# Kernel optimization log

Measured on AMD Instinct MI355X. Metric: run time of the kernel, lower is better.

## Reference

```python
import jax, jax.numpy as jnp
import numpy as np

D = 128        # feature_dims
ITERS = 2      # update_iters
B, R = 8, 256  # n segments (proteins), residues per segment
NEG_SLOPE = 0.1

def leaky(x):
    return jax.nn.leaky_relu(x, NEG_SLOPE)

def setup_inputs() -> dict:
    key = jax.random.key(0)
    ks = jax.random.split(key, 13)
    def w(k, shape):
        fan_in = shape[0]
        return jax.random.normal(k, shape, jnp.float32) / np.sqrt(fan_in)
    return {
        "fresidues": jax.random.normal(ks[0], (B, R, 20), jnp.float32),
        "coordinates": jax.random.normal(ks[1], (B, R, 3), jnp.float32) * 10.0,
        "W_emb": w(ks[2], (20, D)),                    # res_embedding (no bias)
        "W_e1": w(ks[3], (2 * D + 1, D)),              # linear_e layer 1
        "b_e1": jnp.zeros((D,), jnp.float32),
        "W_e2": w(ks[4], (D, D)),                      # linear_e layer 2
        "b_e2": jnp.zeros((D,), jnp.float32),
        "W_inf": w(ks[5], (D, 1)),                     # linear_inf gate
        "b_inf": jnp.zeros((1,), jnp.float32),
        "W_h1": w(ks[6], (2 * D, D)),                  # linear_h layer 1
        "b_h1": jnp.zeros((D,), jnp.float32),
        "W_h2": w(ks[7], (D, D)),                      # linear_h layer 2
        "b_h2": jnp.zeros((D,), jnp.float32),
    }

def reference(fresidues, coordinates, W_emb, W_e1, b_e1, W_e2, b_e2,
              W_inf, b_inf, W_h1, b_h1, W_h2, b_h2):
    # h: [B,R,D]
    h = leaky(fresidues @ W_emb)
    # pairwise squared distances: [B,R,R,1], constant across iterations
    d2 = jnp.sum(jnp.square(coordinates[:, :, None, :] - coordinates[:, None, :, :]),
                 axis=-1, keepdims=True)
    # mask out self-edges (1 - eye): [1,R,R,1]
    mask = (1.0 - jnp.eye(R, dtype=h.dtype))[None, :, :, None]
    # split edge-MLP first-layer weights to avoid materializing the [B,R,R,2D+1] concat:
    # m_input = cat([h_i, h_j, d2]) @ W_e1  ==  h_i@W_i + h_j@W_j + d2*w_d
    W_i, W_j, w_d = W_e1[:D], W_e1[D:2 * D], W_e1[2 * D]
    for _ in range(ITERS):
        ti = h @ W_i                                   # [B,R,D] receiver part
        tj = h @ W_j                                   # [B,R,D] sender part
        pre = ti[:, :, None, :] + tj[:, None, :, :] + d2 * w_d + b_e1  # [B,R,R,D]
        m = leaky(leaky(pre) @ W_e2 + b_e2)            # [B,R,R,D]
        e = jax.nn.sigmoid(m @ W_inf + b_inf) * mask   # [B,R,R,1]
        m_pre = jnp.sum(m * e, axis=2)                 # sum over senders j -> [B,R,D]
        hm = jnp.concatenate([h, m_pre], axis=-1)      # [B,R,2D]
        h = (leaky(hm @ W_h1 + b_h1) @ W_h2 + b_h2) + h
    return h

if __name__ == "__main__":
    out = reference(**setup_inputs())
    print(out.shape, out.dtype)
```

## Files before the change

kernel.cpp:

```cpp
#include <hip/hip_runtime.h>

typedef unsigned short ushort_t;
typedef __attribute__((ext_vector_type(8))) short shortx8;
typedef __attribute__((ext_vector_type(4))) float floatx4;
typedef __attribute__((ext_vector_type(2))) float floatx2;

#define NS 0.1f

__device__ __forceinline__ ushort_t f2bf_rne(float f) {
  union { float f; unsigned int u; } v; v.f = f;
  unsigned int r = v.u + 0x7FFFu + ((v.u >> 16) & 1u);
  return (ushort_t)(r >> 16);
}
__device__ __forceinline__ unsigned int pk2bf(float a, float b) {
  union { float f; unsigned int u; } x, y; x.f = a; y.f = b;
  return __builtin_amdgcn_perm(y.u + 0x8000u, x.u + 0x8000u, 0x07060302u);
}
__device__ __forceinline__ unsigned int cvtpk_bf16(float a, float b) {
  unsigned int r;
  asm("v_cvt_pk_bf16_f32 %0, %1, %2" : "=v"(r) : "v"(a), "v"(b));
  return r;
}
__device__ __forceinline__ ushort_t f2bf_rhu(float f) {
  union { float f; unsigned int u; } v; v.f = f;
  return (ushort_t)((v.u + 0x8000u) >> 16);
}
__device__ __forceinline__ float lk(float x) { return fmaxf(x, NS * x); }
__device__ __forceinline__ floatx2 lk2(floatx2 v) {
  return __builtin_elementwise_max(v, v * (floatx2){NS, NS});
}

__global__ __launch_bounds__(256) void prep_w(
    const float* __restrict__ W_e1, const float* __restrict__ W_e2,
    const float* __restrict__ W_h1, const float* __restrict__ W_h2,
    ushort_t* __restrict__ wijf, ushort_t* __restrict__ we2f,
    ushort_t* __restrict__ wh1f, ushort_t* __restrict__ wh2f) {
  int e = blockIdx.x * 256 + threadIdx.x;
  int which, le;
  if (e < 32768) { which = 0; le = e; }
  else if (e < 49152) { which = 1; le = e - 32768; }
  else if (e < 81920) { which = 2; le = e - 49152; }
  else { which = 3; le = e - 81920; }
  const int NT = (which == 0) ? 16 : 8;
  int f = le >> 3, j = le & 7;
  int lane = f & 63, ft = f >> 6;
  int t = ft % NT, s = ft / NT;
  int n = t * 16 + (lane & 15), k = s * 32 + (lane >> 4) * 8 + j;
  float v; ushort_t* d;
  if (which == 0) { v = (n < 128) ? W_e1[k * 128 + n] : W_e1[(128 + k) * 128 + (n - 128)]; d = wijf; }
  else if (which == 1) { v = W_e2[k * 128 + n]; d = we2f; }
  else if (which == 2) { v = W_h1[k * 128 + n]; d = wh1f; }
  else { v = W_h2[k * 128 + n]; d = wh2f; }
  d[le] = f2bf_rne(v);
}

__device__ __forceinline__ void proj_store(float v, int m, int n,
                                           float* __restrict__ ti, float* __restrict__ tjf) {
  if (n < 128) {
    ti[(size_t)m * 128 + n] = v;
  } else {
    int k = n - 128, b = m >> 8, j = m & 255;
    int s = k >> 5, lg2 = (k >> 3) & 3, j8 = k & 7;
    tjf[((((size_t)(b * 4 + s)) * 256 + j) * 4 + lg2) * 8 + j8] = v;
  }
}

__global__ __launch_bounds__(256) void h0_proj(
    const float* __restrict__ fres, const float* __restrict__ Wemb,
    const ushort_t* __restrict__ wijf, float* __restrict__ h_out,
    float* __restrict__ ti, float* __restrict__ tjf) {
  const int m0 = blockIdx.x * 16;
  const int tid = threadIdx.x;
  const int w = tid >> 6, lane = tid & 63, l16 = lane & 15, lg = lane >> 4;
  __shared__ __align__(16) ushort_t sH[16][136];
  {
    const int row = tid >> 4, c0 = (tid & 15) * 8;
    const float* fr = fres + (size_t)(m0 + row) * 20;
    float a[8] = {0, 0, 0, 0, 0, 0, 0, 0};
    for (int k = 0; k < 20; ++k) {
      float fv = fr[k];
      float4 w0 = *(const float4*)(Wemb + k * 128 + c0);
      float4 w1 = *(const float4*)(Wemb + k * 128 + c0 + 4);
      a[0] += fv * w0.x; a[1] += fv * w0.y; a[2] += fv * w0.z; a[3] += fv * w0.w;
      a[4] += fv * w1.x; a[5] += fv * w1.y; a[6] += fv * w1.z; a[7] += fv * w1.w;
    }
#pragma unroll
    for (int x = 0; x < 8; ++x) a[x] = lk(a[x]);
    float* ho = h_out + (size_t)(m0 + row) * 128 + c0;
    *(float4*)ho = (float4){a[0], a[1], a[2], a[3]};
    *(float4*)(ho + 4) = (float4){a[4], a[5], a[6], a[7]};
    unsigned int* sh = (unsigned int*)&sH[row][c0];
    sh[0] = pk2bf(a[0], a[1]); sh[1] = pk2bf(a[2], a[3]);
    sh[2] = pk2bf(a[4], a[5]); sh[3] = pk2bf(a[6], a[7]);
  }
  __syncthreads();
  floatx4 ap[4];
#pragma unroll
  for (int q = 0; q < 4; ++q) ap[q] = (floatx4){0.f, 0.f, 0.f, 0.f};
  const shortx8* Wp = (const shortx8*)wijf;
#pragma unroll
  for (int s = 0; s < 4; ++s) {
    shortx8 af = *(const shortx8*)&sH[l16][s * 32 + lg * 8];
#pragma unroll
    for (int q = 0; q < 4; ++q)
      ap[q] = __builtin_amdgcn_mfma_f32_16x16x32_bf16(af, Wp[(s * 16 + 4 * w + q) * 64 + lane], ap[q], 0, 0, 0);
  }
#pragma unroll
  for (int q = 0; q < 4; ++q) {
    const int n = (4 * w + q) * 16 + l16;
#pragma unroll
    for (int r = 0; r < 4; ++r) proj_store(ap[q][r], m0 + lg * 4 + r, n, ti, tjf);
  }
}

__global__ __launch_bounds__(512, 4) void edge_kernel(
    const float* __restrict__ ti, const float* __restrict__ tjf,
    const float* __restrict__ coords, const ushort_t* __restrict__ we2f,
    const float* __restrict__ W_e1, const float* __restrict__ b_e1,
    const float* __restrict__ b_e2, const float* __restrict__ W_inf,
    const float* __restrict__ b_inf, float* __restrict__ mp) {
  const int blk = blockIdx.x;
  const int b = blk >> 8, i = blk & 255;
  const int tid = threadIdx.x;
  const int w = tid >> 6, lane = tid & 63, l16 = lane & 15, lg = lane >> 4;

  __shared__ __align__(16) ushort_t sW[16384];
  __shared__ __align__(16) float sTiP[128];
  __shared__ __align__(16) float sWd[128];
  __shared__ __align__(16) float sD2[256];
  __shared__ __align__(16) float sMp[8][128];

  {
    shortx8* dst = (shortx8*)sW;
    const shortx8* src = (const shortx8*)we2f;
#pragma unroll
    for (int r = 0; r < 4; ++r) dst[r * 512 + tid] = src[r * 512 + tid];
  }
  if (tid < 128) {
    sTiP[tid] = ti[(size_t)(b * 256 + i) * 128 + tid] + b_e1[tid];
    sWd[tid] = W_e1[256 * 128 + tid];
  } else if (tid >= 256) {
    const int j = tid - 256;
    float dx = coords[(size_t)(b * 256 + i) * 3 + 0] - coords[(size_t)(b * 256 + j) * 3 + 0];
    float dy = coords[(size_t)(b * 256 + i) * 3 + 1] - coords[(size_t)(b * 256 + j) * 3 + 1];
    float dz = coords[(size_t)(b * 256 + i) * 3 + 2] - coords[(size_t)(b * 256 + j) * 3 + 2];
    sD2[j] = dx * dx + dy * dy + dz * dz;
  }
  floatx4 acc[2][8];
#pragma unroll
  for (int t = 0; t < 8; ++t) {
    float bv = b_e2[t * 16 + l16];
    acc[0][t] = (floatx4){bv, bv, bv, bv};
    acc[1][t] = acc[0][t];
  }
  __syncthreads();

  float d2a[2];
  d2a[0] = sD2[w * 16 + l16];
  d2a[1] = sD2[128 + w * 16 + l16];
  const shortx8* sWf = (const shortx8*)sW;

#pragma unroll
  for (int s = 0; s < 4; ++s) {
    const int k0 = s * 32 + lg * 8;
    floatx2 p2[4], w2[4];
#pragma unroll
    for (int x = 0; x < 4; ++x) {
      p2[x] = *(const floatx2*)&sTiP[k0 + 2 * x];
      w2[x] = *(const floatx2*)&sWd[k0 + 2 * x];
    }
    shortx8 af[2];
#pragma unroll
    for (int c = 0; c < 2; ++c) {
      const int jr = c * 128 + w * 16 + l16;
      const float* tb = tjf + (((size_t)(b * 4 + s) * 256 + jr) * 4 + lg) * 8;
      float4 t0 = *(const float4*)tb;
      float4 t1 = *(const float4*)(tb + 4);
      const floatx2 d2v = (floatx2){d2a[c], d2a[c]};
      floatx2 l0 = lk2((floatx2){t0.x, t0.y} + (p2[0] + d2v * w2[0]));
      floatx2 l1 = lk2((floatx2){t0.z, t0.w} + (p2[1] + d2v * w2[1]));
      floatx2 l2 = lk2((floatx2){t1.x, t1.y} + (p2[2] + d2v * w2[2]));
      floatx2 l3 = lk2((floatx2){t1.z, t1.w} + (p2[3] + d2v * w2[3]));
      union { shortx8 s8; unsigned int u[4]; } A;
      A.u[0] = cvtpk_bf16(l0.x, l0.y); A.u[1] = cvtpk_bf16(l1.x, l1.y);
      A.u[2] = cvtpk_bf16(l2.x, l2.y); A.u[3] = cvtpk_bf16(l3.x, l3.y);
      af[c] = A.s8;
    }
#pragma unroll
    for (int tg = 0; tg < 2; ++tg) {
      shortx8 b0 = sWf[(s * 8 + tg * 4 + 0) * 64 + lane];
      shortx8 b1 = sWf[(s * 8 + tg * 4 + 1) * 64 + lane];
      shortx8 b2 = sWf[(s * 8 + tg * 4 + 2) * 64 + lane];
      shortx8 b3 = sWf[(s * 8 + tg * 4 + 3) * 64 + lane];
      __builtin_amdgcn_s_setprio(1);
#pragma unroll
      for (int c = 0; c < 2; ++c) {
        acc[c][tg * 4 + 0] = __builtin_amdgcn_mfma_f32_16x16x32_bf16(af[c], b0, acc[c][tg * 4 + 0], 0, 0, 0);
        acc[c][tg * 4 + 1] = __builtin_amdgcn_mfma_f32_16x16x32_bf16(af[c], b1, acc[c][tg * 4 + 1], 0, 0, 0);
        acc[c][tg * 4 + 2] = __builtin_amdgcn_mfma_f32_16x16x32_bf16(af[c], b2, acc[c][tg * 4 + 2], 0, 0, 0);
        acc[c][tg * 4 + 3] = __builtin_amdgcn_mfma_f32_16x16x32_bf16(af[c], b3, acc[c][tg * 4 + 3], 0, 0, 0);
      }
      __builtin_amdgcn_s_setprio(0);
    }
  }

  float winfv[8], mpacc[8];
#pragma unroll
  for (int t = 0; t < 8; ++t) { winfv[t] = W_inf[t * 16 + l16]; mpacc[t] = 0.f; }
  const float binf = b_inf[0];
#pragma unroll
  for (int c = 0; c < 2; ++c) {
#pragma unroll
    for (int t = 0; t < 8; ++t) {
      floatx2 v0 = lk2((floatx2){acc[c][t][0], acc[c][t][1]});
      floatx2 v1 = lk2((floatx2){acc[c][t][2], acc[c][t][3]});
      acc[c][t][0] = v0.x; acc[c][t][1] = v0.y; acc[c][t][2] = v1.x; acc[c][t][3] = v1.y;
    }
    float p[4];
#pragma unroll
    for (int r = 0; r < 4; ++r) {
      float sum = 0.f;
#pragma unroll
      for (int t = 0; t < 8; ++t) sum += acc[c][t][r] * winfv[t];
      p[r] = sum;
    }
#pragma unroll
    for (int off = 1; off <= 8; off <<= 1)
#pragma unroll
      for (int r = 0; r < 4; ++r) p[r] += __shfl_xor(p[r], off);
#pragma unroll
    for (int r = 0; r < 4; ++r) {
      const int jg = c * 128 + w * 16 + lg * 4 + r;
      float x = p[r] + binf;
      float e = __builtin_amdgcn_rcpf(1.f + __expf(-x));
      if (jg == i) e = 0.f;
#pragma unroll
      for (int t = 0; t < 8; ++t) mpacc[t] += acc[c][t][r] * e;
    }
  }
#pragma unroll
  for (int t = 0; t < 8; ++t) {
    mpacc[t] += __shfl_xor(mpacc[t], 16);
    mpacc[t] += __shfl_xor(mpacc[t], 32);
  }
  if (lg == 0) {
#pragma unroll
    for (int t = 0; t < 8; ++t) sMp[w][t * 16 + l16] = mpacc[t];
  }
  __syncthreads();
  if (tid < 128) {
    float v = sMp[0][tid] + sMp[1][tid] + sMp[2][tid] + sMp[3][tid]
            + sMp[4][tid] + sMp[5][tid] + sMp[6][tid] + sMp[7][tid];
    mp[(size_t)(b * 256 + i) * 128 + tid] = v;
  }
}

__global__ __launch_bounds__(256) void node_kernel(
    const float* __restrict__ h_in, const float* __restrict__ mp,
    const ushort_t* __restrict__ wh1f, const float* __restrict__ b_h1,
    const ushort_t* __restrict__ wh2f, const float* __restrict__ b_h2,
    const ushort_t* __restrict__ wijf, float* __restrict__ h_out,
    float* __restrict__ ti, float* __restrict__ tjf, const int do_proj) {
  const int m0 = blockIdx.x * 16;
  const int tid = threadIdx.x;
  const int w = tid >> 6, lane = tid & 63, l16 = lane & 15, lg = lane >> 4;
  __shared__ __align__(16) ushort_t sA[16][264];
  __shared__ __align__(16) ushort_t sU[16][136];
  __shared__ __align__(16) ushort_t sHp[16][136];

  {
    const int row = tid >> 4, c0 = (tid & 15) * 16;
    unsigned int* dst = (unsigned int*)&sA[row][c0];
    if (c0 < 128) {
      const float* src = h_in + (size_t)(m0 + row) * 128 + c0;
#pragma unroll
      for (int x = 0; x < 8; ++x) dst[x] = pk2bf(src[2 * x], src[2 * x + 1]);
    } else {
      const float* s0 = mp + (size_t)(m0 + row) * 128 + (c0 - 128);
#pragma unroll
      for (int x = 0; x < 8; ++x) dst[x] = pk2bf(s0[2 * x], s0[2 * x + 1]);
    }
  }
  __syncthreads();
  floatx4 au[2];
#pragma unroll
  for (int q = 0; q < 2; ++q) { float bv = b_h1[(2 * w + q) * 16 + l16]; au[q] = (floatx4){bv, bv, bv, bv}; }
  const shortx8* W1 = (const shortx8*)wh1f;
#pragma unroll
  for (int s = 0; s < 8; ++s) {
    shortx8 af = *(const shortx8*)&sA[l16][s * 32 + lg * 8];
#pragma unroll
    for (int q = 0; q < 2; ++q)
      au[q] = __builtin_amdgcn_mfma_f32_16x16x32_bf16(af, W1[(s * 8 + 2 * w + q) * 64 + lane], au[q], 0, 0, 0);
  }
#pragma unroll
  for (int q = 0; q < 2; ++q)
#pragma unroll
    for (int r = 0; r < 4; ++r)
      sU[lg * 4 + r][(2 * w + q) * 16 + l16] = f2bf_rhu(lk(au[q][r]));
  __syncthreads();
  floatx4 ah[2];
#pragma unroll
  for (int q = 0; q < 2; ++q) { float bv = b_h2[(2 * w + q) * 16 + l16]; ah[q] = (floatx4){bv, bv, bv, bv}; }
  const shortx8* W2 = (const shortx8*)wh2f;
#pragma unroll
  for (int s = 0; s < 4; ++s) {
    shortx8 af = *(const shortx8*)&sU[l16][s * 32 + lg * 8];
#pragma unroll
    for (int q = 0; q < 2; ++q)
      ah[q] = __builtin_amdgcn_mfma_f32_16x16x32_bf16(af, W2[(s * 8 + 2 * w + q) * 64 + lane], ah[q], 0, 0, 0);
  }
#pragma unroll
  for (int q = 0; q < 2; ++q) {
    const int n = (2 * w + q) * 16 + l16;
#pragma unroll
    for (int r = 0; r < 4; ++r) {
      const int m = m0 + lg * 4 + r;
      float v = ah[q][r] + h_in[(size_t)m * 128 + n];
      h_out[(size_t)m * 128 + n] = v;
      sHp[lg * 4 + r][n] = f2bf_rhu(v);
    }
  }
  if (!do_proj) return;
  __syncthreads();
  floatx4 ap[4];
#pragma unroll
  for (int q = 0; q < 4; ++q) ap[q] = (floatx4){0.f, 0.f, 0.f, 0.f};
  const shortx8* Wp = (const shortx8*)wijf;
#pragma unroll
  for (int s = 0; s < 4; ++s) {
    shortx8 af = *(const shortx8*)&sHp[l16][s * 32 + lg * 8];
#pragma unroll
    for (int q = 0; q < 4; ++q)
      ap[q] = __builtin_amdgcn_mfma_f32_16x16x32_bf16(af, Wp[(s * 16 + 4 * w + q) * 64 + lane], ap[q], 0, 0, 0);
  }
#pragma unroll
  for (int q = 0; q < 4; ++q) {
    const int n = (4 * w + q) * 16 + l16;
#pragma unroll
    for (int r = 0; r < 4; ++r) proj_store(ap[q][r], m0 + lg * 4 + r, n, ti, tjf);
  }
}

extern "C" void kernel_launch(void* const* d_in, const int* in_sizes, int n_in,
                              void* d_out, int out_size, void* d_ws, size_t ws_size,
                              hipStream_t stream) {
  const float* fres   = (const float*)d_in[0];
  const float* coords = (const float*)d_in[1];
  const float* W_emb  = (const float*)d_in[2];
  const float* W_e1   = (const float*)d_in[3];
  const float* b_e1   = (const float*)d_in[4];
  const float* W_e2   = (const float*)d_in[5];
  const float* b_e2   = (const float*)d_in[6];
  const float* W_inf  = (const float*)d_in[7];
  const float* b_inf  = (const float*)d_in[8];
  const float* W_h1   = (const float*)d_in[9];
  const float* b_h1   = (const float*)d_in[10];
  const float* W_h2   = (const float*)d_in[11];
  const float* b_h2   = (const float*)d_in[12];
  float* out = (float*)d_out;

  char* ws = (char*)d_ws;
  float* hA  = (float*)(ws + (0 << 20));
  float* hB  = (float*)(ws + (1 << 20));
  float* tib = (float*)(ws + (2 << 20));
  float* tjf = (float*)(ws + (3 << 20));
  float* mpb = (float*)(ws + (4 << 20));
  ushort_t* wijf = (ushort_t*)(ws + (6 << 20));
  ushort_t* we2f = wijf + 32768;
  ushort_t* wh1f = we2f + 16384;
  ushort_t* wh2f = wh1f + 32768;

  prep_w<<<384, 256, 0, stream>>>(W_e1, W_e2, W_h1, W_h2, wijf, we2f, wh1f, wh2f);
  h0_proj<<<128, 256, 0, stream>>>(fres, W_emb, wijf, hA, tib, tjf);

  edge_kernel<<<2048, 512, 0, stream>>>(tib, tjf, coords, we2f, W_e1, b_e1, b_e2, W_inf, b_inf, mpb);
  node_kernel<<<128, 256, 0, stream>>>(hA, mpb, wh1f, b_h1, wh2f, b_h2, wijf, hB, tib, tjf, 1);

  edge_kernel<<<2048, 512, 0, stream>>>(tib, tjf, coords, we2f, W_e1, b_e1, b_e2, W_inf, b_inf, mpb);
  node_kernel<<<128, 256, 0, stream>>>(hB, mpb, wh1f, b_h1, wh2f, b_h2, wijf, out, tib, tjf, 0);
}
```

Baseline: 180.9 us.

## Process four receiver rows per edge block with double-buffered per-row setup

```diff
diff --git a/kernel.cpp b/kernel.cpp
--- a/kernel.cpp
+++ b/kernel.cpp
@@ -28,6 +28,19 @@
 __device__ __forceinline__ float lk(float x) { return fmaxf(x, NS * x); }
 __device__ __forceinline__ floatx2 lk2(floatx2 v) {
   return __builtin_elementwise_max(v, v * (floatx2){NS, NS});
+}
+
+__device__ __forceinline__ float row16_sum(float x) {
+  int t;
+  t = __builtin_amdgcn_update_dpp(0, __builtin_bit_cast(int, x), 0x128, 0xF, 0xF, true);
+  x += __builtin_bit_cast(float, t);
+  t = __builtin_amdgcn_update_dpp(0, __builtin_bit_cast(int, x), 0x124, 0xF, 0xF, true);
+  x += __builtin_bit_cast(float, t);
+  t = __builtin_amdgcn_update_dpp(0, __builtin_bit_cast(int, x), 0x4E, 0xF, 0xF, true);
+  x += __builtin_bit_cast(float, t);
+  t = __builtin_amdgcn_update_dpp(0, __builtin_bit_cast(int, x), 0xB1, 0xF, 0xF, true);
+  x += __builtin_bit_cast(float, t);
+  return x;
 }
 
 __global__ __launch_bounds__(256) void prep_w(
@@ -120,14 +133,16 @@
     const float* __restrict__ b_e2, const float* __restrict__ W_inf,
     const float* __restrict__ b_inf, float* __restrict__ mp) {
   const int blk = blockIdx.x;
-  const int b = blk >> 8, i = blk & 255;
+  const int gi0 = blk << 2;
+  const int b = gi0 >> 8, i0 = gi0 & 255;
   const int tid = threadIdx.x;
   const int w = tid >> 6, lane = tid & 63, l16 = lane & 15, lg = lane >> 4;
 
   __shared__ __align__(16) ushort_t sW[16384];
-  __shared__ __align__(16) float sTiP[128];
+  __shared__ __align__(16) float sTiP[2][128];
+  __shared__ __align__(16) float sD2[2][256];
   __shared__ __align__(16) float sWd[128];
-  __shared__ __align__(16) float sD2[256];
+  __shared__ __align__(16) float sC[3][256];
   __shared__ __align__(16) float sMp[8][128];
 
   {
@@ -136,122 +151,139 @@
 #pragma unroll
     for (int r = 0; r < 4; ++r) dst[r * 512 + tid] = src[r * 512 + tid];
   }
+  if (tid < 256) {
+    sC[0][tid] = coords[(size_t)(b * 256 + tid) * 3 + 0];
+    sC[1][tid] = coords[(size_t)(b * 256 + tid) * 3 + 1];
+    sC[2][tid] = coords[(size_t)(b * 256 + tid) * 3 + 2];
+  }
   if (tid < 128) {
-    sTiP[tid] = ti[(size_t)(b * 256 + i) * 128 + tid] + b_e1[tid];
     sWd[tid] = W_e1[256 * 128 + tid];
+    sTiP[0][tid] = ti[(size_t)(b * 256 + i0) * 128 + tid] + b_e1[tid];
   } else if (tid >= 256) {
     const int j = tid - 256;
-    float dx = coords[(size_t)(b * 256 + i) * 3 + 0] - coords[(size_t)(b * 256 + j) * 3 + 0];
-    float dy = coords[(size_t)(b * 256 + i) * 3 + 1] - coords[(size_t)(b * 256 + j) * 3 + 1];
-    float dz = coords[(size_t)(b * 256 + i) * 3 + 2] - coords[(size_t)(b * 256 + j) * 3 + 2];
-    sD2[j] = dx * dx + dy * dy + dz * dz;
-  }
-  floatx4 acc[2][8];
-#pragma unroll
-  for (int t = 0; t < 8; ++t) {
-    float bv = b_e2[t * 16 + l16];
-    acc[0][t] = (floatx4){bv, bv, bv, bv};
-    acc[1][t] = acc[0][t];
+    float dx = coords[(size_t)(b * 256 + i0) * 3 + 0] - coords[(size_t)(b * 256 + j) * 3 + 0];
+    float dy = coords[(size_t)(b * 256 + i0) * 3 + 1] - coords[(size_t)(b * 256 + j) * 3 + 1];
+    float dz = coords[(size_t)(b * 256 + i0) * 3 + 2] - coords[(size_t)(b * 256 + j) * 3 + 2];
+    sD2[0][j] = dx * dx + dy * dy + dz * dz;
   }
   __syncthreads();
 
-  float d2a[2];
-  d2a[0] = sD2[w * 16 + l16];
-  d2a[1] = sD2[128 + w * 16 + l16];
   const shortx8* sWf = (const shortx8*)sW;
 
-#pragma unroll
-  for (int s = 0; s < 4; ++s) {
-    const int k0 = s * 32 + lg * 8;
-    floatx2 p2[4], w2[4];
-#pragma unroll
-    for (int x = 0; x < 4; ++x) {
-      p2[x] = *(const floatx2*)&sTiP[k0 + 2 * x];
-      w2[x] = *(const floatx2*)&sWd[k0 + 2 * x];
-    }
-    shortx8 af[2];
+  for (int it = 0; it < 4; ++it) {
+    const int i = i0 + it;
+    const int bu = it & 1;
+
+    floatx4 acc[2][8];
+#pragma unroll
+    for (int t = 0; t < 8; ++t) {
+      float bv = b_e2[t * 16 + l16];
+      acc[0][t] = (floatx4){bv, bv, bv, bv};
+      acc[1][t] = acc[0][t];
+    }
+    float d2a[2];
+    d2a[0] = sD2[bu][w * 16 + l16];
+    d2a[1] = sD2[bu][128 + w * 16 + l16];
+
+#pragma unroll
+    for (int s = 0; s < 4; ++s) {
+      const int k0 = s * 32 + lg * 8;
+      floatx2 p2[4], w2[4];
+#pragma unroll
+      for (int x = 0; x < 4; ++x) {
+        p2[x] = *(const floatx2*)&sTiP[bu][k0 + 2 * x];
+        w2[x] = *(const floatx2*)&sWd[k0 + 2 * x];
+      }
+      shortx8 af[2];
+#pragma unroll
+      for (int c = 0; c < 2; ++c) {
+        const int jr = c * 128 + w * 16 + l16;
+        const float* tb = tjf + (((size_t)(b * 4 + s) * 256 + jr) * 4 + lg) * 8;
+        float4 t0 = *(const float4*)tb;
+        float4 t1 = *(const float4*)(tb + 4);
+        const floatx2 d2v = (floatx2){d2a[c], d2a[c]};
+        floatx2 l0 = lk2((floatx2){t0.x, t0.y} + (p2[0] + d2v * w2[0]));
+        floatx2 l1 = lk2((floatx2){t0.z, t0.w} + (p2[1] + d2v * w2[1]));
+        floatx2 l2 = lk2((floatx2){t1.x, t1.y} + (p2[2] + d2v * w2[2]));
+        floatx2 l3 = lk2((floatx2){t1.z, t1.w} + (p2[3] + d2v * w2[3]));
+        union { shortx8 s8; unsigned int u[4]; } A;
+        A.u[0] = cvtpk_bf16(l0.x, l0.y); A.u[1] = cvtpk_bf16(l1.x, l1.y);
+        A.u[2] = cvtpk_bf16(l2.x, l2.y); A.u[3] = cvtpk_bf16(l3.x, l3.y);
+        af[c] = A.s8;
+      }
+#pragma unroll
+      for (int tg = 0; tg < 2; ++tg) {
+        shortx8 b0 = sWf[(s * 8 + tg * 4 + 0) * 64 + lane];
+        shortx8 b1 = sWf[(s * 8 + tg * 4 + 1) * 64 + lane];
+        shortx8 b2 = sWf[(s * 8 + tg * 4 + 2) * 64 + lane];
+        shortx8 b3 = sWf[(s * 8 + tg * 4 + 3) * 64 + lane];
+        __builtin_amdgcn_s_setprio(1);
+#pragma unroll
+        for (int c = 0; c < 2; ++c) {
+          acc[c][tg * 4 + 0] = __builtin_amdgcn_mfma_f32_16x16x32_bf16(af[c], b0, acc[c][tg * 4 + 0], 0, 0, 0);
+          acc[c][tg * 4 + 1] = __builtin_amdgcn_mfma_f32_16x16x32_bf16(af[c], b1, acc[c][tg * 4 + 1], 0, 0, 0);
+          acc[c][tg * 4 + 2] = __builtin_amdgcn_mfma_f32_16x16x32_bf16(af[c], b2, acc[c][tg * 4 + 2], 0, 0, 0);
+          acc[c][tg * 4 + 3] = __builtin_amdgcn_mfma_f32_16x16x32_bf16(af[c], b3, acc[c][tg * 4 + 3], 0, 0, 0);
+        }
+        __builtin_amdgcn_s_setprio(0);
+      }
+    }
+
+    if (it < 3) {
+      const int i2 = i0 + it + 1;
+      if (tid < 128) {
+        sTiP[bu ^ 1][tid] = ti[(size_t)(b * 256 + i2) * 128 + tid] + b_e1[tid];
+      } else if (tid >= 256) {
+        const int j = tid - 256;
+        float dx = sC[0][i2] - sC[0][j];
+        float dy = sC[1][i2] - sC[1][j];
+        float dz = sC[2][i2] - sC[2][j];
+        sD2[bu ^ 1][j] = dx * dx + dy * dy + dz * dz;
+      }
+    }
+
+    float winfv[8], mpacc[8];
+#pragma unroll
+    for (int t = 0; t < 8; ++t) { winfv[t] = W_inf[t * 16 + l16]; mpacc[t] = 0.f; }
+    const float binf = b_inf[0];
 #pragma unroll
     for (int c = 0; c < 2; ++c) {
-      const int jr = c * 128 + w * 16 + l16;
-      const float* tb = tjf + (((size_t)(b * 4 + s) * 256 + jr) * 4 + lg) * 8;
-      float4 t0 = *(const float4*)tb;
-      float4 t1 = *(const float4*)(tb + 4);
-      const floatx2 d2v = (floatx2){d2a[c], d2a[c]};
-      floatx2 l0 = lk2((floatx2){t0.x, t0.y} + (p2[0] + d2v * w2[0]));
-      floatx2 l1 = lk2((floatx2){t0.z, t0.w} + (p2[1] + d2v * w2[1]));
-      floatx2 l2 = lk2((floatx2){t1.x, t1.y} + (p2[2] + d2v * w2[2]));
-      floatx2 l3 = lk2((floatx2){t1.z, t1.w} + (p2[3] + d2v * w2[3]));
-      union { shortx8 s8; unsigned int u[4]; } A;
-      A.u[0] = cvtpk_bf16(l0.x, l0.y); A.u[1] = cvtpk_bf16(l1.x, l1.y);
-      A.u[2] = cvtpk_bf16(l2.x, l2.y); A.u[3] = cvtpk_bf16(l3.x, l3.y);
-      af[c] = A.s8;
-    }
-#pragma unroll
-    for (int tg = 0; tg < 2; ++tg) {
-      shortx8 b0 = sWf[(s * 8 + tg * 4 + 0) * 64 + lane];
-      shortx8 b1 = sWf[(s * 8 + tg * 4 + 1) * 64 + lane];
-      shortx8 b2 = sWf[(s * 8 + tg * 4 + 2) * 64 + lane];
-      shortx8 b3 = sWf[(s * 8 + tg * 4 + 3) * 64 + lane];
-      __builtin_amdgcn_s_setprio(1);
-#pragma unroll
-      for (int c = 0; c < 2; ++c) {
-        acc[c][tg * 4 + 0] = __builtin_amdgcn_mfma_f32_16x16x32_bf16(af[c], b0, acc[c][tg * 4 + 0], 0, 0, 0);
-        acc[c][tg * 4 + 1] = __builtin_amdgcn_mfma_f32_16x16x32_bf16(af[c], b1, acc[c][tg * 4 + 1], 0, 0, 0);
-        acc[c][tg * 4 + 2] = __builtin_amdgcn_mfma_f32_16x16x32_bf16(af[c], b2, acc[c][tg * 4 + 2], 0, 0, 0);
-        acc[c][tg * 4 + 3] = __builtin_amdgcn_mfma_f32_16x16x32_bf16(af[c], b3, acc[c][tg * 4 + 3], 0, 0, 0);
-      }
-      __builtin_amdgcn_s_setprio(0);
-    }
-  }
-
-  float winfv[8], mpacc[8];
-#pragma unroll
-  for (int t = 0; t < 8; ++t) { winfv[t] = W_inf[t * 16 + l16]; mpacc[t] = 0.f; }
-  const float binf = b_inf[0];
-#pragma unroll
-  for (int c = 0; c < 2; ++c) {
+#pragma unroll
+      for (int t = 0; t < 8; ++t) {
+        floatx2 v0 = lk2((floatx2){acc[c][t][0], acc[c][t][1]});
+        floatx2 v1 = lk2((floatx2){acc[c][t][2], acc[c][t][3]});
+        acc[c][t][0] = v0.x; acc[c][t][1] = v0.y; acc[c][t][2] = v1.x; acc[c][t][3] = v1.y;
+      }
+#pragma unroll
+      for (int r = 0; r < 4; ++r) {
+        float sum = 0.f;
+#pragma unroll
+        for (int t = 0; t < 8; ++t) sum += acc[c][t][r] * winfv[t];
+        sum = row16_sum(sum);
+        const int jg = c * 128 + w * 16 + lg * 4 + r;
+        float x = sum + binf;
+        float e = __builtin_amdgcn_rcpf(1.f + __expf(-x));
+        if (jg == i) e = 0.f;
+#pragma unroll
+        for (int t = 0; t < 8; ++t) mpacc[t] += acc[c][t][r] * e;
+      }
+    }
 #pragma unroll
     for (int t = 0; t < 8; ++t) {
-      floatx2 v0 = lk2((floatx2){acc[c][t][0], acc[c][t][1]});
-      floatx2 v1 = lk2((floatx2){acc[c][t][2], acc[c][t][3]});
-      acc[c][t][0] = v0.x; acc[c][t][1] = v0.y; acc[c][t][2] = v1.x; acc[c][t][3] = v1.y;
-    }
-    float p[4];
-#pragma unroll
-    for (int r = 0; r < 4; ++r) {
-      float sum = 0.f;
-#pragma unroll
-      for (int t = 0; t < 8; ++t) sum += acc[c][t][r] * winfv[t];
-      p[r] = sum;
-    }
-#pragma unroll
-    for (int off = 1; off <= 8; off <<= 1)
-#pragma unroll
-      for (int r = 0; r < 4; ++r) p[r] += __shfl_xor(p[r], off);
-#pragma unroll
-    for (int r = 0; r < 4; ++r) {
-      const int jg = c * 128 + w * 16 + lg * 4 + r;
-      float x = p[r] + binf;
-      float e = __builtin_amdgcn_rcpf(1.f + __expf(-x));
-      if (jg == i) e = 0.f;
-#pragma unroll
-      for (int t = 0; t < 8; ++t) mpacc[t] += acc[c][t][r] * e;
-    }
-  }
-#pragma unroll
-  for (int t = 0; t < 8; ++t) {
-    mpacc[t] += __shfl_xor(mpacc[t], 16);
-    mpacc[t] += __shfl_xor(mpacc[t], 32);
-  }
-  if (lg == 0) {
-#pragma unroll
-    for (int t = 0; t < 8; ++t) sMp[w][t * 16 + l16] = mpacc[t];
-  }
-  __syncthreads();
-  if (tid < 128) {
-    float v = sMp[0][tid] + sMp[1][tid] + sMp[2][tid] + sMp[3][tid]
-            + sMp[4][tid] + sMp[5][tid] + sMp[6][tid] + sMp[7][tid];
-    mp[(size_t)(b * 256 + i) * 128 + tid] = v;
+      mpacc[t] += __shfl_xor(mpacc[t], 16);
+      mpacc[t] += __shfl_xor(mpacc[t], 32);
+    }
+    if (lg == 0) {
+#pragma unroll
+      for (int t = 0; t < 8; ++t) sMp[w][t * 16 + l16] = mpacc[t];
+    }
+    __syncthreads();
+    if (tid < 128) {
+      float v = sMp[0][tid] + sMp[1][tid] + sMp[2][tid] + sMp[3][tid]
+              + sMp[4][tid] + sMp[5][tid] + sMp[6][tid] + sMp[7][tid];
+      mp[(size_t)(b * 256 + i) * 128 + tid] = v;
+    }
+    __syncthreads();
   }
 }
 
@@ -374,9 +406,9 @@
   prep_w<<<384, 256, 0, stream>>>(W_e1, W_e2, W_h1, W_h2, wijf, we2f, wh1f, wh2f);
   h0_proj<<<128, 256, 0, stream>>>(fres, W_emb, wijf, hA, tib, tjf);
 
-  edge_kernel<<<2048, 512, 0, stream>>>(tib, tjf, coords, we2f, W_e1, b_e1, b_e2, W_inf, b_inf, mpb);
+  edge_kernel<<<512, 512, 0, stream>>>(tib, tjf, coords, we2f, W_e1, b_e1, b_e2, W_inf, b_inf, mpb);
   node_kernel<<<128, 256, 0, stream>>>(hA, mpb, wh1f, b_h1, wh2f, b_h2, wijf, hB, tib, tjf, 1);
 
-  edge_kernel<<<2048, 512, 0, stream>>>(tib, tjf, coords, we2f, W_e1, b_e1, b_e2, W_inf, b_inf, mpb);
+  edge_kernel<<<512, 512, 0, stream>>>(tib, tjf, coords, we2f, W_e1, b_e1, b_e2, W_inf, b_inf, mpb);
   node_kernel<<<128, 256, 0, stream>>>(hB, mpb, wh1f, b_h1, wh2f, b_h2, wijf, out, tib, tjf, 0);
 }
```

After: 232.4 us. 28.5% more time.
